# Kernel tuning notes

Hardware: AMD Instinct MI355X
Metric: run time of the kernel (lower is better)

Reference implementation:

```python
import jax, jax.numpy as jnp
import numpy as np

B, T, N, D, H, F, L, V = 4, 512, 1024, 384, 8, 1536, 6, 8000
HD = D // H


def _pe(t, d):
    pos = np.arange(t)[:, None].astype(np.float32)
    div = np.exp(np.arange(0, d, 2).astype(np.float32) * (-np.log(10000.0) / d))
    pe = np.zeros((t, d), np.float32)
    pe[:, 0::2] = np.sin(pos * div)
    pe[:, 1::2] = np.cos(pos * div)
    return jnp.asarray(pe)


def _ln(x, g, b, eps=1e-5):
    m = jnp.mean(x, -1, keepdims=True)
    v = jnp.mean((x - m) ** 2, -1, keepdims=True)
    return (x - m) * jax.lax.rsqrt(v + eps) * g + b


def _mha(xq, xkv, qw, qb, kw, kb, vw, vb, ow, ob, causal):
    Bq, Tq, Dm = xq.shape
    Nk = xkv.shape[1]

    def proj(x, w, b):
        return (x @ w + b).reshape(x.shape[0], x.shape[1], H, HD).transpose(0, 2, 1, 3)

    q, k, v = proj(xq, qw, qb), proj(xkv, kw, kb), proj(xkv, vw, vb)
    s = jnp.einsum('bhtd,bhnd->bhtn', q, k) * (HD ** -0.5)
    if causal:  # triu(ones(T, T_total), diagonal=1) since T_total == T (no cache)
        mask = jnp.triu(jnp.ones((Tq, Nk), bool), 1)
        s = jnp.where(mask, -jnp.inf, s)
    p = jax.nn.softmax(s, -1)
    o = jnp.einsum('bhtn,bhnd->bhtd', p, v).transpose(0, 2, 1, 3).reshape(Bq, Tq, Dm)
    return o @ ow + ob


def setup_inputs() -> dict:
    key = jax.random.key(0)
    ks = iter(jax.random.split(key, 40))
    w = lambda shape, s=0.02: jax.random.normal(next(ks), shape, jnp.float32) * s
    inp = {
        'encoder_out': jax.random.normal(next(ks), (B, N, D), jnp.float32),
        'emb': w((V, D)),
    }
    for p in ('sa', 'ca'):
        for n in ('q', 'k', 'v', 'o'):
            inp[f'{p}_{n}w'] = w((L, D, D))
            inp[f'{p}_{n}b'] = jnp.zeros((L, D), jnp.float32)
    for n in ('ln1', 'ln2', 'ln3'):
        inp[f'{n}_g'] = jnp.ones((L, D), jnp.float32)
        inp[f'{n}_b'] = jnp.zeros((L, D), jnp.float32)
    inp['ffn_w1'] = w((L, D, F)); inp['ffn_b1'] = jnp.zeros((L, F), jnp.float32)
    inp['ffn_w2'] = w((L, F, D)); inp['ffn_b2'] = jnp.zeros((L, D), jnp.float32)
    inp['on_g'] = jnp.ones((D,), jnp.float32); inp['on_b'] = jnp.zeros((D,), jnp.float32)
    inp['out_w'] = w((D, V)); inp['out_b'] = jnp.zeros((V,), jnp.float32)
    inp['target_ids'] = jax.random.randint(next(ks), (B, T), 0, V)
    return inp


def _forward(encoder_out, emb, sa_qw, sa_qb, sa_kw, sa_kb, sa_vw, sa_vb, sa_ow, sa_ob,
             ca_qw, ca_qb, ca_kw, ca_kb, ca_vw, ca_vb, ca_ow, ca_ob,
             ln1_g, ln1_b, ln2_g, ln2_b, ln3_g, ln3_b,
             ffn_w1, ffn_b1, ffn_w2, ffn_b2, on_g, on_b, out_w, out_b, target_ids):
    x = emb[target_ids] + _pe(T, D)[None]  # [B,T,D]
    for i in range(L):
        a = _mha(x, x, sa_qw[i], sa_qb[i], sa_kw[i], sa_kb[i], sa_vw[i], sa_vb[i], sa_ow[i], sa_ob[i], True)
        x = _ln(x + a, ln1_g[i], ln1_b[i])
        c = _mha(x, encoder_out, ca_qw[i], ca_qb[i], ca_kw[i], ca_kb[i], ca_vw[i], ca_vb[i], ca_ow[i], ca_ob[i], False)
        x = _ln(x + c, ln2_g[i], ln2_b[i])
        h = jax.nn.gelu(x @ ffn_w1[i] + ffn_b1[i], approximate=False) @ ffn_w2[i] + ffn_b2[i]
        x = _ln(x + h, ln3_g[i], ln3_b[i])
    x = _ln(x, on_g, on_b)
    return x @ out_w + out_b  # logits [B,T,V]


def reference(encoder_out, emb, sa_qw, sa_qb, sa_kw, sa_kb, sa_vw, sa_vb, sa_ow, sa_ob,
              ca_qw, ca_qb, ca_kw, ca_kb, ca_vw, ca_vb, ca_ow, ca_ob,
              ln1_g, ln1_b, ln2_g, ln2_b, ln3_g, ln3_b,
              ffn_w1, ffn_b1, ffn_w2, ffn_b2, on_g, on_b, out_w, out_b, target_ids):
    return _forward(encoder_out, emb, sa_qw, sa_qb, sa_kw, sa_kb, sa_vw, sa_vb, sa_ow, sa_ob,
                    ca_qw, ca_qb, ca_kw, ca_kb, ca_vw, ca_vb, ca_ow, ca_ob,
                    ln1_g, ln1_b, ln2_g, ln2_b, ln3_g, ln3_b,
                    ffn_w1, ffn_b1, ffn_w2, ffn_b2, on_g, on_b, out_w, out_b, target_ids)
```

## Files before the change

### kernel.cpp

```cpp
#include <hip/hip_runtime.h>
#include <hip/hip_bf16.h>
#include <math.h>

typedef __hip_bfloat16 bf16;
typedef __attribute__((ext_vector_type(8))) short short8;
typedef __attribute__((ext_vector_type(4))) float f32x4;
typedef __attribute__((ext_vector_type(4))) unsigned short us4;

#define Bc 4
#define Tc 512
#define Nc 1024
#define Dc 384
#define Hc 8
#define Fc 1536
#define Lc 6
#define Vc 8000
#define HDc 48

__device__ __forceinline__ float ldsel(const void* p, long long i, int isbf) {
  return isbf ? __bfloat162float(((const bf16*)p)[i]) : ((const float*)p)[i];
}
__device__ __forceinline__ void stsel(void* p, long long i, float v, int isbf) {
  if (isbf) ((bf16*)p)[i] = __float2bfloat16(v);
  else      ((float*)p)[i] = v;
}
__device__ __forceinline__ unsigned short f2bf(float x) {
  unsigned int u = __float_as_uint(x);
  return (unsigned short)((u + 0x7fffu + ((u >> 16) & 1u)) >> 16);
}

__global__ void detect_kernel(const unsigned int* __restrict__ g,
                              int* __restrict__ flag) {
  if (threadIdx.x == 0 && blockIdx.x == 0)
    *flag = (g[0] == 0x3F803F80u) ? 1 : 0;
}

__global__ __launch_bounds__(256) void wt_kernel(
    const void* __restrict__ in, bf16* __restrict__ out, int K, int N,
    long long outStride, const int* __restrict__ flagp) {
  const int isbf = *flagp;
  __shared__ float t[32][33];
  const long long cin = (long long)blockIdx.z * K * N;
  const long long cout = (long long)blockIdx.z * outStride;
  const int n0 = blockIdx.x * 32, k0 = blockIdx.y * 32;
  const int tx = threadIdx.x, ty = threadIdx.y;
#pragma unroll
  for (int r = 0; r < 4; ++r)
    t[ty * 4 + r][tx] =
        ldsel(in, cin + (long long)(k0 + ty * 4 + r) * N + n0 + tx, isbf);
  __syncthreads();
#pragma unroll
  for (int r = 0; r < 4; ++r)
    out[cout + (long long)(n0 + ty * 4 + r) * K + k0 + tx] =
        __float2bfloat16(t[tx][ty * 4 + r]);
}

__global__ __launch_bounds__(256) void cvt_kernel(
    const void* __restrict__ in, bf16* __restrict__ out,
    const int* __restrict__ flagp) {
  const int isbf = *flagp;
  const long long i = ((long long)blockIdx.x * 256 + threadIdx.x) * 4;
  if (isbf) {
    *(us4*)((unsigned short*)out + i) = *(const us4*)((const unsigned short*)in + i);
  } else {
    float4 v = *(const float4*)((const float*)in + i);
    unsigned short* o = (unsigned short*)out + i;
    o[0] = f2bf(v.x); o[1] = f2bf(v.y); o[2] = f2bf(v.z); o[3] = f2bf(v.w);
  }
}

__global__ __launch_bounds__(256) void bfuse_kernel(
    const void* __restrict__ b0, const void* __restrict__ b1,
    const void* __restrict__ b2, float* __restrict__ out, int nseg,
    const int* __restrict__ flagp) {
  const int isbf = *flagp;
  const int i = blockIdx.x;
  for (int n = threadIdx.x; n < Dc; n += 256) {
    out[(long long)i * nseg * Dc + n] = ldsel(b0, (long long)i * Dc + n, isbf);
    if (nseg > 1)
      out[(long long)i * nseg * Dc + Dc + n] = ldsel(b1, (long long)i * Dc + n, isbf);
    if (nseg > 2)
      out[(long long)i * nseg * Dc + 2 * Dc + n] = ldsel(b2, (long long)i * Dc + n, isbf);
  }
}

__global__ __launch_bounds__(256) void mgemm_kernel(
    const bf16* __restrict__ A, const void* __restrict__ B, long long bOff,
    const void* __restrict__ bias, long long biasOff, void* __restrict__ C,
    int M, int N, int K, int cMode, int act, int biasBf, int bT,
    const int* __restrict__ flagp) {
  const int isbf = *flagp;
  const int cbf = (cMode == 2) ? isbf : cMode;
  const int bbf = (biasBf == 2) ? isbf : biasBf;

  __shared__ __align__(16) unsigned short As[64][72];
  __shared__ __align__(16) unsigned short Bs[64][72];

  const int tid = threadIdx.x;
  const int m0 = blockIdx.x * 64, n0 = blockIdx.y * 64;
  const int lane = tid & 63, wv = tid >> 6;
  const int fr = lane & 15;
  const int fk = (lane >> 4) * 8;

  const int sr = tid >> 2;
  const int sk = (tid & 3) * 16;

  f32x4 acc[4] = {};

  if (bT == 0) {
    const bf16* Bp = (const bf16*)B + bOff;
    const bf16* Ar = A + (long long)(m0 + sr) * K + sk;
    const bf16* Br = Bp + (long long)(n0 + sr) * K + sk;
    short8 a0 = *(const short8*)(Ar);
    short8 a1 = *(const short8*)(Ar + 8);
    short8 b0 = *(const short8*)(Br);
    short8 b1 = *(const short8*)(Br + 8);
    for (int k0 = 0; k0 < K; k0 += 64) {
      *(short8*)(&As[sr][sk]) = a0;
      *(short8*)(&As[sr][sk + 8]) = a1;
      *(short8*)(&Bs[sr][sk]) = b0;
      *(short8*)(&Bs[sr][sk + 8]) = b1;
      __syncthreads();
      if (k0 + 64 < K) {
        a0 = *(const short8*)(Ar + k0 + 64);
        a1 = *(const short8*)(Ar + k0 + 72);
        b0 = *(const short8*)(Br + k0 + 64);
        b1 = *(const short8*)(Br + k0 + 72);
      }
#pragma unroll
      for (int ks = 0; ks < 64; ks += 32) {
        short8 a = *(const short8*)(&As[16 * wv + fr][ks + fk]);
#pragma unroll
        for (int j = 0; j < 4; ++j) {
          short8 b = *(const short8*)(&Bs[16 * j + fr][ks + fk]);
          acc[j] = __builtin_amdgcn_mfma_f32_16x16x32_bf16(a, b, acc[j], 0, 0, 0);
        }
      }
      __syncthreads();
    }
  } else {
    const int bk = tid >> 2;
    const int bn = (tid & 3) * 16;
    for (int k0 = 0; k0 < K; k0 += 64) {
      {
        const long long off = (long long)(m0 + sr) * K + k0 + sk;
        const short8* p = (const short8*)(A + off);
        *(short8*)(&As[sr][sk]) = p[0];
        *(short8*)(&As[sr][sk + 8]) = p[1];
      }
      const long long off = bOff + (long long)(k0 + bk) * N + n0 + bn;
      if (isbf) {
        const short8* p = (const short8*)((const bf16*)B + off);
        short8 v0 = p[0], v1 = p[1];
#pragma unroll
        for (int j = 0; j < 8; ++j) {
          Bs[bn + j][bk] = (unsigned short)v0[j];
          Bs[bn + 8 + j][bk] = (unsigned short)v1[j];
        }
      } else {
        const float4* p = (const float4*)((const float*)B + off);
        float4 f0 = p[0], f1 = p[1], f2 = p[2], f3 = p[3];
        Bs[bn + 0][bk] = f2bf(f0.x);  Bs[bn + 1][bk] = f2bf(f0.y);
        Bs[bn + 2][bk] = f2bf(f0.z);  Bs[bn + 3][bk] = f2bf(f0.w);
        Bs[bn + 4][bk] = f2bf(f1.x);  Bs[bn + 5][bk] = f2bf(f1.y);
        Bs[bn + 6][bk] = f2bf(f1.z);  Bs[bn + 7][bk] = f2bf(f1.w);
        Bs[bn + 8][bk] = f2bf(f2.x);  Bs[bn + 9][bk] = f2bf(f2.y);
        Bs[bn + 10][bk] = f2bf(f2.z); Bs[bn + 11][bk] = f2bf(f2.w);
        Bs[bn + 12][bk] = f2bf(f3.x); Bs[bn + 13][bk] = f2bf(f3.y);
        Bs[bn + 14][bk] = f2bf(f3.z); Bs[bn + 15][bk] = f2bf(f3.w);
      }
      __syncthreads();
#pragma unroll
      for (int ks = 0; ks < 64; ks += 32) {
        short8 a = *(const short8*)(&As[16 * wv + fr][ks + fk]);
#pragma unroll
        for (int j = 0; j < 4; ++j) {
          short8 b = *(const short8*)(&Bs[16 * j + fr][ks + fk]);
          acc[j] = __builtin_amdgcn_mfma_f32_16x16x32_bf16(a, b, acc[j], 0, 0, 0);
        }
      }
      __syncthreads();
    }
  }

#pragma unroll
  for (int j = 0; j < 4; ++j) {
    const int col = n0 + 16 * j + fr;
    float bv = bias ? ldsel(bias, biasOff + col, bbf) : 0.f;
#pragma unroll
    for (int q = 0; q < 4; ++q) {
      const int row = m0 + 16 * wv + (lane >> 4) * 4 + q;
      float v = acc[j][q] + bv;
      if (act == 1) v = 0.5f * v * (1.f + erff(v * 0.70710678118654752f));
      stsel(C, (long long)row * N + col, v, cbf);
    }
  }
}

__global__ __launch_bounds__(256) void mattn_kernel(
    const bf16* __restrict__ Qb, int ldq, const bf16* __restrict__ Kb,
    const bf16* __restrict__ Vb, int ldkv, int kvRows,
    float* __restrict__ PO, float* __restrict__ Mb, float* __restrict__ Lb,
    int Nk, int causal) {
  const int bh = blockIdx.y;
  const int b = bh >> 3, h = bh & 7;
  const int row0 = blockIdx.x * 64;
  const int z = blockIdx.z;
  const int tid = threadIdx.x;
  const int lane = tid & 63, wv = tid >> 6;
  const int fr = lane & 15, g = lane >> 4;
  const int fk = g * 8, g4 = g * 4;
  const int rbase = row0 + wv * 16 + g4;

  __shared__ __align__(16) unsigned short Ks[64][72];
  __shared__ __align__(16) unsigned short Vt[48][72];
  __shared__ __align__(16) unsigned short Ps[4][16][72];

  for (int i = tid; i < 64 * 16; i += 256) Ks[i >> 4][48 + (i & 15)] = 0;

  const int qrow = row0 + wv * 16 + fr;
  const bf16* Qp = Qb + (long long)(b * Tc + qrow) * ldq + h * HDc;
  short8 q0 = *(const short8*)(Qp + fk);
  short8 q1 = {};
  if (g < 2) q1 = *(const short8*)(Qp + 32 + fk);

  const bf16* Kp = Kb + (long long)b * kvRows * ldkv + h * HDc;
  const bf16* Vp = Vb + (long long)b * kvRows * ldkv + h * HDc;

  const int c0 = tid, c1 = 256 + tid;
  const int r0 = c0 / 6, o0 = (c0 % 6) * 8;
  const int r1 = c1 / 6, o1 = (c1 % 6) * 8;
  const bool has1 = (tid < 128);

  const int nT = causal ? (blockIdx.x + 1) : (Nk >> 6);
  const int tlo = (nT * z) >> 1, thi = (nT * (z + 1)) >> 1;

  float m[4] = {-3e38f, -3e38f, -3e38f, -3e38f};
  float l[4] = {0.f, 0.f, 0.f, 0.f};
  f32x4 oa[3] = {};

  short8 kA = {}, vA = {}, kB = {}, vB = {};
  if (tlo < thi) {
    const long long nb = (long long)tlo * 64;
    kA = *(const short8*)(Kp + (nb + r0) * ldkv + o0);
    vA = *(const short8*)(Vp + (nb + r0) * ldkv + o0);
    if (has1) {
      kB = *(const short8*)(Kp + (nb + r1) * ldkv + o1);
      vB = *(const short8*)(Vp + (nb + r1) * ldkv + o1);
    }
  }

  const float scale = 0.14433756729740643f;

  for (int t = tlo; t < thi; ++t) {
    *(short8*)&Ks[r0][o0] = kA;
#pragma unroll
    for (int j = 0; j < 8; ++j) Vt[o0 + j][r0] = (unsigned short)vA[j];
    if (has1) {
      *(short8*)&Ks[r1][o1] = kB;
#pragma unroll
      for (int j = 0; j < 8; ++j) Vt[o1 + j][r1] = (unsigned short)vB[j];
    }
    __syncthreads();

    if (t + 1 < thi) {
      const long long nb = (long long)(t + 1) * 64;
      kA = *(const short8*)(Kp + (nb + r0) * ldkv + o0);
      vA = *(const short8*)(Vp + (nb + r0) * ldkv + o0);
      if (has1) {
        kB = *(const short8*)(Kp + (nb + r1) * ldkv + o1);
        vB = *(const short8*)(Vp + (nb + r1) * ldkv + o1);
      }
    }

    f32x4 s[4] = {};
#pragma unroll
    for (int tt = 0; tt < 4; ++tt) {
      short8 b0 = *(const short8*)&Ks[16 * tt + fr][fk];
      short8 b1 = *(const short8*)&Ks[16 * tt + fr][32 + fk];
      s[tt] = __builtin_amdgcn_mfma_f32_16x16x32_bf16(q0, b0, s[tt], 0, 0, 0);
      s[tt] = __builtin_amdgcn_mfma_f32_16x16x32_bf16(q1, b1, s[tt], 0, 0, 0);
    }

    const int n0 = t * 64;
#pragma unroll
    for (int tt = 0; tt < 4; ++tt) {
      const int n = n0 + 16 * tt + fr;
#pragma unroll
      for (int q = 0; q < 4; ++q) {
        float v = s[tt][q] * scale;
        if (causal && n > rbase + q) v = -3e38f;
        s[tt][q] = v;
      }
    }

#pragma unroll
    for (int q = 0; q < 4; ++q) {
      float tm = fmaxf(fmaxf(s[0][q], s[1][q]), fmaxf(s[2][q], s[3][q]));
      tm = fmaxf(tm, __shfl_xor(tm, 1, 64));
      tm = fmaxf(tm, __shfl_xor(tm, 2, 64));
      tm = fmaxf(tm, __shfl_xor(tm, 4, 64));
      tm = fmaxf(tm, __shfl_xor(tm, 8, 64));
      const float mn = fmaxf(m[q], tm);
      const float f = expf(m[q] - mn);
      float rs = 0.f;
#pragma unroll
      for (int tt = 0; tt < 4; ++tt) {
        float p = expf(s[tt][q] - mn);
        s[tt][q] = p;
        rs += p;
      }
      rs += __shfl_xor(rs, 1, 64);
      rs += __shfl_xor(rs, 2, 64);
      rs += __shfl_xor(rs, 4, 64);
      rs += __shfl_xor(rs, 8, 64);
      l[q] = l[q] * f + rs;
      m[q] = mn;
      oa[0][q] *= f;
      oa[1][q] *= f;
      oa[2][q] *= f;
    }

#pragma unroll
    for (int tt = 0; tt < 4; ++tt)
#pragma unroll
      for (int q = 0; q < 4; ++q)
        Ps[wv][g4 + q][16 * tt + fr] = f2bf(s[tt][q]);

#pragma unroll
    for (int ks = 0; ks < 64; ks += 32) {
      short8 a = *(const short8*)&Ps[wv][fr][ks + fk];
#pragma unroll
      for (int jd = 0; jd < 3; ++jd) {
        short8 bv = *(const short8*)&Vt[16 * jd + fr][ks + fk];
        oa[jd] = __builtin_amdgcn_mfma_f32_16x16x32_bf16(a, bv, oa[jd], 0, 0, 0);
      }
    }
    __syncthreads();
  }

#pragma unroll
  for (int q = 0; q < 4; ++q) {
    float* pp = PO + (long long)(z * (Bc * Tc) + b * Tc + rbase + q) * Dc + h * HDc;
#pragma unroll
    for (int jd = 0; jd < 3; ++jd) pp[16 * jd + fr] = oa[jd][q];
    if (fr == 0) {
      const int mi = z * (Bc * Hc * Tc) + (bh << 9) + rbase + q;
      Mb[mi] = m[q];
      Lb[mi] = l[q];
    }
  }
}

__global__ __launch_bounds__(384) void acomb_kernel(
    const float* __restrict__ PO, const float* __restrict__ Mb,
    const float* __restrict__ Lb, bf16* __restrict__ ATT) {
  const int row = blockIdx.x;
  const int d = threadIdx.x;
  const int b = row >> 9, t = row & 511;
  const int h = d / HDc;
  const int mi = ((b << 3) + h) * Tc + t;
  const float m0 = Mb[mi], m1 = Mb[Bc * Hc * Tc + mi];
  const float l0 = Lb[mi], l1 = Lb[Bc * Hc * Tc + mi];
  const float M = fmaxf(m0, m1);
  const float w0 = expf(m0 - M), w1 = expf(m1 - M);
  const float L = w0 * l0 + w1 * l1;
  const float o = (w0 * PO[(long long)row * Dc + d] +
                   w1 * PO[(long long)(Bc * Tc + row) * Dc + d]) / L;
  ATT[(long long)row * Dc + d] = __float2bfloat16(o);
}

__global__ __launch_bounds__(256) void ln_kernel(
    const float* __restrict__ X, const float* __restrict__ R,
    const void* __restrict__ g, const void* __restrict__ bta, long long gOff,
    void* __restrict__ Y, int yMode, bf16* __restrict__ Yb,
    const int* __restrict__ flagp) {
  const int isbf = *flagp;
  long long row = blockIdx.x;
  int tid = threadIdx.x;
  const float* xr = X + row * Dc;
  const float* rr = R ? R + row * Dc : nullptr;
  float v0 = xr[tid] + (rr ? rr[tid] : 0.f);
  float v1 = 0.f;
  if (tid < 128) v1 = xr[256 + tid] + (rr ? rr[256 + tid] : 0.f);
  __shared__ float red[256];
  red[tid] = v0 + v1;
  __syncthreads();
  for (int s = 128; s > 0; s >>= 1) {
    if (tid < s) red[tid] += red[tid + s];
    __syncthreads();
  }
  float mean = red[0] * (1.f / 384.f);
  __syncthreads();
  float d0 = v0 - mean;
  float d1 = (tid < 128) ? (v1 - mean) : 0.f;
  red[tid] = d0 * d0 + d1 * d1;
  __syncthreads();
  for (int s = 128; s > 0; s >>= 1) {
    if (tid < s) red[tid] += red[tid + s];
    __syncthreads();
  }
  float rstd = rsqrtf(red[0] * (1.f / 384.f) + 1e-5f);
  long long yoff = row * Dc;
  float y0 = d0 * rstd * ldsel(g, gOff + tid, isbf) + ldsel(bta, gOff + tid, isbf);
  stsel(Y, yoff + tid, y0, yMode);
  if (Yb) Yb[yoff + tid] = __float2bfloat16(y0);
  if (tid < 128) {
    float y1 = d1 * rstd * ldsel(g, gOff + 256 + tid, isbf) +
               ldsel(bta, gOff + 256 + tid, isbf);
    stsel(Y, yoff + 256 + tid, y1, yMode);
    if (Yb) Yb[yoff + 256 + tid] = __float2bfloat16(y1);
  }
}

__global__ __launch_bounds__(384) void embed_kernel(
    const void* __restrict__ emb, const int* __restrict__ ids,
    float* __restrict__ X, bf16* __restrict__ Xb,
    const int* __restrict__ flagp) {
  const int isbf = *flagp;
  long long row = blockIdx.x;
  int t = (int)(row % Tc);
  int d = threadIdx.x;
  int id = ids[row];
  float e = ldsel(emb, (long long)id * Dc + d, isbf);
  int i2 = d & ~1;
  float div = expf((float)i2 * (-9.210340371976184f / 384.f));
  float ang = (float)t * div;
  float pe = (d & 1) ? cosf(ang) : sinf(ang);
  float v = e + pe;
  X[row * Dc + d] = v;
  Xb[row * Dc + d] = __float2bfloat16(v);
}

extern "C" void kernel_launch(void* const* d_in, const int* in_sizes, int n_in,
                              void* d_out, int out_size, void* d_ws,
                              size_t ws_size, hipStream_t stream) {
  (void)in_sizes; (void)n_in; (void)out_size;

  const void* enc = d_in[0];
  const void* emb = d_in[1];
  const void* sa_w[4]; const void* sa_b[4];
  for (int j = 0; j < 4; ++j) { sa_w[j] = d_in[2 + 2 * j]; sa_b[j] = d_in[3 + 2 * j]; }
  const void* ca_w[4]; const void* ca_b[4];
  for (int j = 0; j < 4; ++j) { ca_w[j] = d_in[10 + 2 * j]; ca_b[j] = d_in[11 + 2 * j]; }
  const void* ln_g[3]; const void* ln_b[3];
  for (int j = 0; j < 3; ++j) { ln_g[j] = d_in[18 + 2 * j]; ln_b[j] = d_in[19 + 2 * j]; }
  const void* fw1 = d_in[24];
  const void* fb1 = d_in[25];
  const void* fw2 = d_in[26];
  const void* fb2 = d_in[27];
  const void* ong = d_in[28];
  const void* onb = d_in[29];
  const void* outw = d_in[30];
  const void* outb = d_in[31];
  const int* ids = (const int*)d_in[32];

  char* ob = (char*)d_out;
  float* X   = (float*)ob;
  bf16* Xb   = (bf16*)(ob + 3145728);
  float* AO  = (float*)(ob + 4718592);
  bf16* QKV  = (bf16*)(ob + 7864320);
  bf16* KVca = (bf16*)(ob + 12582912);
  bf16* ATT  = (bf16*)(ob + 18874368);
  bf16* HID  = (bf16*)(ob + 20447232);
  float* PO  = (float*)(ob + 20447232);
  float* Mb  = (float*)(ob + 26738688);
  float* Lb  = (float*)(ob + 26869760);
  bf16* encB = (bf16*)(ob + 27000832);
  float* bQKV = (float*)(ob + 30146560);
  float* bKVc = (float*)(ob + 30174208);

  bf16* Y = (bf16*)d_ws;
  int* flag = (int*)((char*)d_ws + 1572864);

  const bool bigws = (ws_size >= (size_t)36028672);
  char* wtb = (char*)d_ws + 1573120;
  bf16* saQKVT = (bf16*)(wtb + 0);
  bf16* saOT   = (bf16*)(wtb + 5308416);
  bf16* caQT   = (bf16*)(wtb + 7077888);
  bf16* caKVT  = (bf16*)(wtb + 8847360);
  bf16* caOT   = (bf16*)(wtb + 12386304);
  bf16* f1T    = (bf16*)(wtb + 14155776);
  bf16* f2T    = (bf16*)(wtb + 21233664);
  bf16* outT   = (bf16*)(wtb + 28311552);

  const int BT = Bc * Tc;
  const int F32 = 0, BF16 = 1, FLAG = 2;

  detect_kernel<<<dim3(1), dim3(64), 0, stream>>>((const unsigned int*)ln_g[0], flag);

  if (bigws) {
    auto wt = [&](const void* in, bf16* out, int K, int N, long long ostr, int C) {
      wt_kernel<<<dim3(N / 32, K / 32, C), dim3(32, 8), 0, stream>>>(
          in, out, K, N, ostr, flag);
    };
    wt(sa_w[0], saQKVT, 384, 384, 1152LL * 384, Lc);
    wt(sa_w[1], saQKVT + 147456, 384, 384, 1152LL * 384, Lc);
    wt(sa_w[2], saQKVT + 294912, 384, 384, 1152LL * 384, Lc);
    wt(sa_w[3], saOT, 384, 384, 147456, Lc);
    wt(ca_w[0], caQT, 384, 384, 147456, Lc);
    wt(ca_w[1], caKVT, 384, 384, 294912, Lc);
    wt(ca_w[2], caKVT + 147456, 384, 384, 294912, Lc);
    wt(ca_w[3], caOT, 384, 384, 147456, Lc);
    wt(fw1, f1T, 384, 1536, 589824, Lc);
    wt(fw2, f2T, 1536, 384, 589824, Lc);
    wt(outw, outT, 384, 8000, 0, 1);
    bfuse_kernel<<<dim3(Lc), dim3(256), 0, stream>>>(sa_b[0], sa_b[1], sa_b[2],
                                                     bQKV, 3, flag);
    bfuse_kernel<<<dim3(Lc), dim3(256), 0, stream>>>(ca_b[1], ca_b[2], ca_b[2],
                                                     bKVc, 2, flag);
  }
  cvt_kernel<<<dim3(1536), dim3(256), 0, stream>>>(enc, encB, flag);

  auto gemmT = [&](const bf16* A, const bf16* Bt, long long bOff,
                   const void* bias, long long biasOff, int biasBf, void* C,
                   int M, int N, int K, int cM, int act) {
    mgemm_kernel<<<dim3(M / 64, N / 64), dim3(256), 0, stream>>>(
        A, Bt, bOff, bias, biasOff, C, M, N, K, cM, act, biasBf, 0, flag);
  };
  auto gemmO = [&](const bf16* A, const void* Bo, long long bOff,
                   const void* bias, long long biasOff, void* C,
                   int M, int N, int K, int cM, int act) {
    mgemm_kernel<<<dim3(M / 64, N / 64), dim3(256), 0, stream>>>(
        A, Bo, bOff, bias, biasOff, C, M, N, K, cM, act, FLAG, 1, flag);
  };
  auto ln = [&](const float* Xp, const float* Rp, const void* g,
                const void* b, long long gOff, void* Yp, int yMode, bf16* Yb) {
    ln_kernel<<<dim3(BT), dim3(256), 0, stream>>>(Xp, Rp, g, b, gOff, Yp,
                                                  yMode, Yb, flag);
  };
  auto attn = [&](const bf16* Q, int ldq, const bf16* Kp, const bf16* Vp,
                  int ldkv, int kvRows, int Nk, int causal) {
    mattn_kernel<<<dim3(Tc / 64, Bc * Hc, 2), dim3(256), 0, stream>>>(
        Q, ldq, Kp, Vp, ldkv, kvRows, PO, Mb, Lb, Nk, causal);
    acomb_kernel<<<dim3(BT), dim3(384), 0, stream>>>(PO, Mb, Lb, ATT);
  };

  embed_kernel<<<dim3(BT), dim3(384), 0, stream>>>(emb, ids, X, Xb, flag);

  bf16* Qf = QKV;
  bf16* Kf = KVca;
  bf16* Vf = (bf16*)((char*)KVca + 3145728);

  for (int i = 0; i < Lc; ++i) {
    const long long wD = (long long)i * Dc * Dc;
    const long long bD = (long long)i * Dc;

    if (bigws) {
      gemmT(Xb, saQKVT, (long long)i * 1152 * 384, bQKV, (long long)i * 1152,
            F32, QKV, BT, 1152, 384, BF16, 0);
      attn(QKV, 1152, QKV + 384, QKV + 768, 1152, Tc, Tc, 1);
      gemmT(ATT, saOT, wD, sa_b[3], bD, FLAG, AO, BT, Dc, Dc, F32, 0);
    } else {
      gemmO(Xb, sa_w[0], wD, sa_b[0], bD, Qf, BT, Dc, Dc, BF16, 0);
      gemmO(Xb, sa_w[1], wD, sa_b[1], bD, Kf, BT, Dc, Dc, BF16, 0);
      gemmO(Xb, sa_w[2], wD, sa_b[2], bD, Vf, BT, Dc, Dc, BF16, 0);
      attn(Qf, 384, Kf, Vf, 384, Tc, Tc, 1);
      gemmO(ATT, sa_w[3], wD, sa_b[3], bD, AO, BT, Dc, Dc, F32, 0);
    }
    ln(X, AO, ln_g[0], ln_b[0], bD, X, F32, Xb);

    if (bigws) {
      gemmT(Xb, caQT, wD, ca_b[0], bD, FLAG, QKV, BT, Dc, Dc, BF16, 0);
      gemmT(encB, caKVT, (long long)i * 768 * 384, bKVc, (long long)i * 768,
            F32, KVca, Bc * Nc, 768, 384, BF16, 0);
      attn(QKV, 384, KVca, KVca + 384, 768, Nc, Nc, 0);
      gemmT(ATT, caOT, wD, ca_b[3], bD, FLAG, AO, BT, Dc, Dc, F32, 0);
    } else {
      gemmO(Xb, ca_w[0], wD, ca_b[0], bD, Qf, BT, Dc, Dc, BF16, 0);
      gemmO(encB, ca_w[1], wD, ca_b[1], bD, Kf, Bc * Nc, Dc, Dc, BF16, 0);
      gemmO(encB, ca_w[2], wD, ca_b[2], bD, Vf, Bc * Nc, Dc, Dc, BF16, 0);
      attn(Qf, 384, Kf, Vf, 384, Nc, Nc, 0);
      gemmO(ATT, ca_w[3], wD, ca_b[3], bD, AO, BT, Dc, Dc, F32, 0);
    }
    ln(X, AO, ln_g[1], ln_b[1], bD, X, F32, Xb);

    if (bigws) {
      gemmT(Xb, f1T, (long long)i * 1536 * 384, fb1, (long long)i * Fc, FLAG,
            HID, BT, Fc, Dc, BF16, 1 );
      gemmT(HID, f2T, (long long)i * 384 * 1536, fb2, bD, FLAG, AO,
            BT, Dc, Fc, F32, 0);
    } else {
      gemmO(Xb, fw1, (long long)i * Dc * Fc, fb1, (long long)i * Fc, HID,
            BT, Fc, Dc, BF16, 1);
      gemmO(HID, fw2, (long long)i * Fc * Dc, fb2, bD, AO, BT, Dc, Fc, F32, 0);
    }
    ln(X, AO, ln_g[2], ln_b[2], bD, X, F32, Xb);
  }

  ln(X, nullptr, ong, onb, 0, Y, BF16, nullptr);
  if (bigws)
    gemmT(Y, outT, 0, outb, 0, FLAG, d_out, BT, Vc, Dc, FLAG, 0);
  else
    gemmO(Y, outw, 0, outb, 0, d_out, BT, Vc, Dc, FLAG, 0);
}
```

Baseline: 1.058 ms.

## Add 128-row MFMA GEMM, fuse attention combine into O-proj, warp-per-row layernorm

Adds a templated GEMM with 128x128 and 128x64 tiles for the large QKV, cross-attention KV, FFN1 and output projections, giving more data reuse per block. Removes the separate split-KV combine kernel: the output-projection GEMM now merges the two partial attention results while loading its A tile. The attention softmax switches to exp2f with a log2e-scaled constant. LayerNorm is rewritten to use one wavefront per row with shuffle reductions and single-pass mean and variance, which may lose some precision. The combine-fused GEMM recomputes the merge weights per tile and uses the slower scalar LDS path, and the larger tiles launch fewer blocks.

Result: slower. 1.154 ms (+9.0%).

```diff
diff --git a/kernel.cpp b/kernel.cpp
--- a/kernel.cpp
+++ b/kernel.cpp
@@ -84,11 +84,97 @@
   }
 }
 
+template <int BN>
+__global__ __launch_bounds__(256) void mgemm128_kernel(
+    const bf16* __restrict__ A, const bf16* __restrict__ Bt, long long bOff,
+    const void* __restrict__ bias, long long biasOff, void* __restrict__ C,
+    int M, int N, int K, int cMode, int act, int biasBf,
+    const int* __restrict__ flagp) {
+  constexpr int RN = BN / 32;
+  const int isbf = *flagp;
+  const int cbf = (cMode == 2) ? isbf : cMode;
+  const int bbf = (biasBf == 2) ? isbf : biasBf;
+
+  __shared__ __align__(16) unsigned short As[128][72];
+  __shared__ __align__(16) unsigned short Bs[BN][72];
+
+  const int tid = threadIdx.x;
+  const int m0 = blockIdx.x * 128, n0 = blockIdx.y * BN;
+  const int lane = tid & 63, wv = tid >> 6;
+  const int wm = wv >> 1, wn = wv & 1;
+  const int fr = lane & 15;
+  const int fk = (lane >> 4) * 8;
+
+  const int ar = tid >> 3;
+  const int ac = (tid & 7) * 8;
+  const bf16* Ap = A + (long long)(m0 + ar) * K + ac;
+  const bf16* Bp = Bt + bOff + (long long)(n0 + ar) * K + ac;
+
+  short8 pa[4], pb[RN * 2];
+#pragma unroll
+  for (int r = 0; r < 4; ++r) pa[r] = *(const short8*)(Ap + r * 32 * K);
+#pragma unroll
+  for (int r = 0; r < RN * 2; ++r) pb[r] = *(const short8*)(Bp + r * 32 * K);
+
+  f32x4 acc[4][RN] = {};
+
+  for (int k0 = 0; k0 < K; k0 += 64) {
+#pragma unroll
+    for (int r = 0; r < 4; ++r) *(short8*)(&As[ar + 32 * r][ac]) = pa[r];
+#pragma unroll
+    for (int r = 0; r < RN * 2; ++r) *(short8*)(&Bs[ar + 32 * r][ac]) = pb[r];
+    __syncthreads();
+    if (k0 + 64 < K) {
+#pragma unroll
+      for (int r = 0; r < 4; ++r)
+        pa[r] = *(const short8*)(Ap + r * 32 * K + k0 + 64);
+#pragma unroll
+      for (int r = 0; r < RN * 2; ++r)
+        pb[r] = *(const short8*)(Bp + r * 32 * K + k0 + 64);
+    }
+#pragma unroll
+    for (int ks = 0; ks < 64; ks += 32) {
+      short8 af[4];
+#pragma unroll
+      for (int mi = 0; mi < 4; ++mi)
+        af[mi] = *(const short8*)(&As[wm * 64 + mi * 16 + fr][ks + fk]);
+      short8 bg[RN];
+#pragma unroll
+      for (int ni = 0; ni < RN; ++ni)
+        bg[ni] = *(const short8*)(&Bs[wn * (BN / 2) + ni * 16 + fr][ks + fk]);
+#pragma unroll
+      for (int mi = 0; mi < 4; ++mi)
+#pragma unroll
+        for (int ni = 0; ni < RN; ++ni)
+          acc[mi][ni] =
+              __builtin_amdgcn_mfma_f32_16x16x32_bf16(af[mi], bg[ni], acc[mi][ni], 0, 0, 0);
+    }
+    __syncthreads();
+  }
+
+#pragma unroll
+  for (int ni = 0; ni < RN; ++ni) {
+    const int col = n0 + wn * (BN / 2) + ni * 16 + fr;
+    const float bv = bias ? ldsel(bias, biasOff + col, bbf) : 0.f;
+#pragma unroll
+    for (int mi = 0; mi < 4; ++mi) {
+#pragma unroll
+      for (int q = 0; q < 4; ++q) {
+        const int row = m0 + wm * 64 + mi * 16 + (lane >> 4) * 4 + q;
+        float v = acc[mi][ni][q] + bv;
+        if (act == 1) v = 0.5f * v * (1.f + erff(v * 0.70710678118654752f));
+        stsel(C, (long long)row * N + col, v, cbf);
+      }
+    }
+  }
+}
+
 __global__ __launch_bounds__(256) void mgemm_kernel(
     const bf16* __restrict__ A, const void* __restrict__ B, long long bOff,
     const void* __restrict__ bias, long long biasOff, void* __restrict__ C,
     int M, int N, int K, int cMode, int act, int biasBf, int bT,
-    const int* __restrict__ flagp) {
+    const float* __restrict__ POm, const float* __restrict__ Mst,
+    const float* __restrict__ Lst, int comb, const int* __restrict__ flagp) {
   const int isbf = *flagp;
   const int cbf = (cMode == 2) ? isbf : cMode;
   const int bbf = (biasBf == 2) ? isbf : biasBf;
@@ -107,7 +193,7 @@
 
   f32x4 acc[4] = {};
 
-  if (bT == 0) {
+  if (bT == 0 && comb == 0) {
     const bf16* Bp = (const bf16*)B + bOff;
     const bf16* Ar = A + (long long)(m0 + sr) * K + sk;
     const bf16* Br = Bp + (long long)(n0 + sr) * K + sk;
@@ -142,32 +228,62 @@
     const int bk = tid >> 2;
     const int bn = (tid & 3) * 16;
     for (int k0 = 0; k0 < K; k0 += 64) {
-      {
+      if (comb) {
+        const int gm = m0 + sr;
+        const int gk = k0 + sk;
+        const int hh = gk / 48;
+        const int bb = gm >> 9, tt = gm & 511;
+        const int mi = ((bb << 3) + hh) * 512 + tt;
+        const float ma = Mst[mi], mb2 = Mst[16384 + mi];
+        const float la = Lst[mi], lb2 = Lst[16384 + mi];
+        const float MM = fmaxf(ma, mb2);
+        float w0 = exp2f(ma - MM), w1 = exp2f(mb2 - MM);
+        const float invL = 1.f / (w0 * la + w1 * lb2);
+        w0 *= invL; w1 *= invL;
+        const float* p0 = POm + (long long)gm * Dc + gk;
+        const float* p1 = POm + (long long)(2048 + gm) * Dc + gk;
+#pragma unroll
+        for (int e = 0; e < 16; e += 4) {
+          float4 x0 = *(const float4*)(p0 + e);
+          float4 x1 = *(const float4*)(p1 + e);
+          As[sr][sk + e + 0] = f2bf(w0 * x0.x + w1 * x1.x);
+          As[sr][sk + e + 1] = f2bf(w0 * x0.y + w1 * x1.y);
+          As[sr][sk + e + 2] = f2bf(w0 * x0.z + w1 * x1.z);
+          As[sr][sk + e + 3] = f2bf(w0 * x0.w + w1 * x1.w);
+        }
+      } else {
         const long long off = (long long)(m0 + sr) * K + k0 + sk;
         const short8* p = (const short8*)(A + off);
         *(short8*)(&As[sr][sk]) = p[0];
         *(short8*)(&As[sr][sk + 8]) = p[1];
       }
-      const long long off = bOff + (long long)(k0 + bk) * N + n0 + bn;
-      if (isbf) {
+      if (bT == 0) {
+        const long long off = bOff + (long long)(n0 + sr) * K + k0 + sk;
         const short8* p = (const short8*)((const bf16*)B + off);
-        short8 v0 = p[0], v1 = p[1];
-#pragma unroll
-        for (int j = 0; j < 8; ++j) {
-          Bs[bn + j][bk] = (unsigned short)v0[j];
-          Bs[bn + 8 + j][bk] = (unsigned short)v1[j];
+        *(short8*)(&Bs[sr][sk]) = p[0];
+        *(short8*)(&Bs[sr][sk + 8]) = p[1];
+      } else {
+        const long long off = bOff + (long long)(k0 + bk) * N + n0 + bn;
+        if (isbf) {
+          const short8* p = (const short8*)((const bf16*)B + off);
+          short8 v0 = p[0], v1 = p[1];
+#pragma unroll
+          for (int j = 0; j < 8; ++j) {
+            Bs[bn + j][bk] = (unsigned short)v0[j];
+            Bs[bn + 8 + j][bk] = (unsigned short)v1[j];
+          }
+        } else {
+          const float4* p = (const float4*)((const float*)B + off);
+          float4 f0 = p[0], f1 = p[1], f2 = p[2], f3 = p[3];
+          Bs[bn + 0][bk] = f2bf(f0.x);  Bs[bn + 1][bk] = f2bf(f0.y);
+          Bs[bn + 2][bk] = f2bf(f0.z);  Bs[bn + 3][bk] = f2bf(f0.w);
+          Bs[bn + 4][bk] = f2bf(f1.x);  Bs[bn + 5][bk] = f2bf(f1.y);
+          Bs[bn + 6][bk] = f2bf(f1.z);  Bs[bn + 7][bk] = f2bf(f1.w);
+          Bs[bn + 8][bk] = f2bf(f2.x);  Bs[bn + 9][bk] = f2bf(f2.y);
+          Bs[bn + 10][bk] = f2bf(f2.z); Bs[bn + 11][bk] = f2bf(f2.w);
+          Bs[bn + 12][bk] = f2bf(f3.x); Bs[bn + 13][bk] = f2bf(f3.y);
+          Bs[bn + 14][bk] = f2bf(f3.z); Bs[bn + 15][bk] = f2bf(f3.w);
         }
-      } else {
-        const float4* p = (const float4*)((const float*)B + off);
-        float4 f0 = p[0], f1 = p[1], f2 = p[2], f3 = p[3];
-        Bs[bn + 0][bk] = f2bf(f0.x);  Bs[bn + 1][bk] = f2bf(f0.y);
-        Bs[bn + 2][bk] = f2bf(f0.z);  Bs[bn + 3][bk] = f2bf(f0.w);
-        Bs[bn + 4][bk] = f2bf(f1.x);  Bs[bn + 5][bk] = f2bf(f1.y);
-        Bs[bn + 6][bk] = f2bf(f1.z);  Bs[bn + 7][bk] = f2bf(f1.w);
-        Bs[bn + 8][bk] = f2bf(f2.x);  Bs[bn + 9][bk] = f2bf(f2.y);
-        Bs[bn + 10][bk] = f2bf(f2.z); Bs[bn + 11][bk] = f2bf(f2.w);
-        Bs[bn + 12][bk] = f2bf(f3.x); Bs[bn + 13][bk] = f2bf(f3.y);
-        Bs[bn + 14][bk] = f2bf(f3.z); Bs[bn + 15][bk] = f2bf(f3.w);
       }
       __syncthreads();
 #pragma unroll
@@ -250,7 +366,7 @@
     }
   }
 
-  const float scale = 0.14433756729740643f;
+  const float scale = 0.20823509f;
 
   for (int t = tlo; t < thi; ++t) {
     *(short8*)&Ks[r0][o0] = kA;
@@ -302,11 +418,11 @@
       tm = fmaxf(tm, __shfl_xor(tm, 4, 64));
       tm = fmaxf(tm, __shfl_xor(tm, 8, 64));
       const float mn = fmaxf(m[q], tm);
-      const float f = expf(m[q] - mn);
+      const float f = exp2f(m[q] - mn);
       float rs = 0.f;
 #pragma unroll
       for (int tt = 0; tt < 4; ++tt) {
-        float p = expf(s[tt][q] - mn);
+        float p = exp2f(s[tt][q] - mn);
         s[tt][q] = p;
         rs += p;
       }
@@ -352,64 +468,40 @@
   }
 }
 
-__global__ __launch_bounds__(384) void acomb_kernel(
-    const float* __restrict__ PO, const float* __restrict__ Mb,
-    const float* __restrict__ Lb, bf16* __restrict__ ATT) {
-  const int row = blockIdx.x;
-  const int d = threadIdx.x;
-  const int b = row >> 9, t = row & 511;
-  const int h = d / HDc;
-  const int mi = ((b << 3) + h) * Tc + t;
-  const float m0 = Mb[mi], m1 = Mb[Bc * Hc * Tc + mi];
-  const float l0 = Lb[mi], l1 = Lb[Bc * Hc * Tc + mi];
-  const float M = fmaxf(m0, m1);
-  const float w0 = expf(m0 - M), w1 = expf(m1 - M);
-  const float L = w0 * l0 + w1 * l1;
-  const float o = (w0 * PO[(long long)row * Dc + d] +
-                   w1 * PO[(long long)(Bc * Tc + row) * Dc + d]) / L;
-  ATT[(long long)row * Dc + d] = __float2bfloat16(o);
-}
-
-__global__ __launch_bounds__(256) void ln_kernel(
+__global__ __launch_bounds__(256) void lnw_kernel(
     const float* __restrict__ X, const float* __restrict__ R,
     const void* __restrict__ g, const void* __restrict__ bta, long long gOff,
     void* __restrict__ Y, int yMode, bf16* __restrict__ Yb,
     const int* __restrict__ flagp) {
   const int isbf = *flagp;
-  long long row = blockIdx.x;
-  int tid = threadIdx.x;
+  const long long row = blockIdx.x * 4 + (threadIdx.x >> 6);
+  const int lane = threadIdx.x & 63;
   const float* xr = X + row * Dc;
   const float* rr = R ? R + row * Dc : nullptr;
-  float v0 = xr[tid] + (rr ? rr[tid] : 0.f);
-  float v1 = 0.f;
-  if (tid < 128) v1 = xr[256 + tid] + (rr ? rr[256 + tid] : 0.f);
-  __shared__ float red[256];
-  red[tid] = v0 + v1;
-  __syncthreads();
-  for (int s = 128; s > 0; s >>= 1) {
-    if (tid < s) red[tid] += red[tid + s];
-    __syncthreads();
-  }
-  float mean = red[0] * (1.f / 384.f);
-  __syncthreads();
-  float d0 = v0 - mean;
-  float d1 = (tid < 128) ? (v1 - mean) : 0.f;
-  red[tid] = d0 * d0 + d1 * d1;
-  __syncthreads();
-  for (int s = 128; s > 0; s >>= 1) {
-    if (tid < s) red[tid] += red[tid + s];
-    __syncthreads();
-  }
-  float rstd = rsqrtf(red[0] * (1.f / 384.f) + 1e-5f);
-  long long yoff = row * Dc;
-  float y0 = d0 * rstd * ldsel(g, gOff + tid, isbf) + ldsel(bta, gOff + tid, isbf);
-  stsel(Y, yoff + tid, y0, yMode);
-  if (Yb) Yb[yoff + tid] = __float2bfloat16(y0);
-  if (tid < 128) {
-    float y1 = d1 * rstd * ldsel(g, gOff + 256 + tid, isbf) +
-               ldsel(bta, gOff + 256 + tid, isbf);
-    stsel(Y, yoff + 256 + tid, y1, yMode);
-    if (Yb) Yb[yoff + 256 + tid] = __float2bfloat16(y1);
+  float v[6];
+  float s = 0.f, s2 = 0.f;
+#pragma unroll
+  for (int j = 0; j < 6; ++j) {
+    const int d = lane + 64 * j;
+    float x = xr[d] + (rr ? rr[d] : 0.f);
+    v[j] = x; s += x; s2 += x * x;
+  }
+#pragma unroll
+  for (int k = 1; k < 64; k <<= 1) {
+    s += __shfl_xor(s, k, 64);
+    s2 += __shfl_xor(s2, k, 64);
+  }
+  const float mean = s * (1.f / 384.f);
+  const float var = s2 * (1.f / 384.f) - mean * mean;
+  const float rstd = rsqrtf(var + 1e-5f);
+  const long long yo = row * Dc;
+#pragma unroll
+  for (int j = 0; j < 6; ++j) {
+    const int d = lane + 64 * j;
+    float y = (v[j] - mean) * rstd * ldsel(g, gOff + d, isbf) +
+              ldsel(bta, gOff + d, isbf);
+    stsel(Y, yo + d, y, yMode);
+    if (Yb) Yb[yo + d] = __float2bfloat16(y);
   }
 }
 
@@ -461,7 +553,6 @@
   float* AO  = (float*)(ob + 4718592);
   bf16* QKV  = (bf16*)(ob + 7864320);
   bf16* KVca = (bf16*)(ob + 12582912);
-  bf16* ATT  = (bf16*)(ob + 18874368);
   bf16* HID  = (bf16*)(ob + 20447232);
   float* PO  = (float*)(ob + 20447232);
   float* Mb  = (float*)(ob + 26738688);
@@ -512,28 +603,34 @@
   }
   cvt_kernel<<<dim3(1536), dim3(256), 0, stream>>>(enc, encB, flag);
 
-  auto gemmT = [&](const bf16* A, const bf16* Bt, long long bOff,
-                   const void* bias, long long biasOff, int biasBf, void* C,
-                   int M, int N, int K, int cM, int act) {
+  auto gemm128 = [&](const bf16* A, const bf16* Bt, long long bOff,
+                     const void* bias, long long biasOff, int biasBf, void* C,
+                     int M, int N, int K, int cM, int act) {
+    mgemm128_kernel<128><<<dim3(M / 128, N / 128), dim3(256), 0, stream>>>(
+        A, Bt, bOff, bias, biasOff, C, M, N, K, cM, act, biasBf, flag);
+  };
+  auto gemm128n64 = [&](const bf16* A, const bf16* Bt, long long bOff,
+                        const void* bias, long long biasOff, int biasBf,
+                        void* C, int M, int N, int K, int cM, int act) {
+    mgemm128_kernel<64><<<dim3(M / 128, N / 64), dim3(256), 0, stream>>>(
+        A, Bt, bOff, bias, biasOff, C, M, N, K, cM, act, biasBf, flag);
+  };
+  auto gemmOld = [&](const bf16* A, const void* Bo, long long bOff,
+                     const void* bias, long long biasOff, int biasBf, void* C,
+                     int M, int N, int K, int cM, int act, int bT, int comb) {
     mgemm_kernel<<<dim3(M / 64, N / 64), dim3(256), 0, stream>>>(
-        A, Bt, bOff, bias, biasOff, C, M, N, K, cM, act, biasBf, 0, flag);
-  };
-  auto gemmO = [&](const bf16* A, const void* Bo, long long bOff,
-                   const void* bias, long long biasOff, void* C,
-                   int M, int N, int K, int cM, int act) {
-    mgemm_kernel<<<dim3(M / 64, N / 64), dim3(256), 0, stream>>>(
-        A, Bo, bOff, bias, biasOff, C, M, N, K, cM, act, FLAG, 1, flag);
+        A, Bo, bOff, bias, biasOff, C, M, N, K, cM, act, biasBf, bT,
+        PO, Mb, Lb, comb, flag);
   };
   auto ln = [&](const float* Xp, const float* Rp, const void* g,
                 const void* b, long long gOff, void* Yp, int yMode, bf16* Yb) {
-    ln_kernel<<<dim3(BT), dim3(256), 0, stream>>>(Xp, Rp, g, b, gOff, Yp,
-                                                  yMode, Yb, flag);
+    lnw_kernel<<<dim3(BT / 4), dim3(256), 0, stream>>>(Xp, Rp, g, b, gOff, Yp,
+                                                       yMode, Yb, flag);
   };
   auto attn = [&](const bf16* Q, int ldq, const bf16* Kp, const bf16* Vp,
                   int ldkv, int kvRows, int Nk, int causal) {
     mattn_kernel<<<dim3(Tc / 64, Bc * Hc, 2), dim3(256), 0, stream>>>(
         Q, ldq, Kp, Vp, ldkv, kvRows, PO, Mb, Lb, Nk, causal);
-    acomb_kernel<<<dim3(BT), dim3(384), 0, stream>>>(PO, Mb, Lb, ATT);
   };
 
   embed_kernel<<<dim3(BT), dim3(384), 0, stream>>>(emb, ids, X, Xb, flag);
@@ -547,50 +644,51 @@
     const long long bD = (long long)i * Dc;
 
     if (bigws) {
-      gemmT(Xb, saQKVT, (long long)i * 1152 * 384, bQKV, (long long)i * 1152,
-            F32, QKV, BT, 1152, 384, BF16, 0);
+      gemm128(Xb, saQKVT, (long long)i * 1152 * 384, bQKV, (long long)i * 1152,
+              F32, QKV, BT, 1152, 384, BF16, 0);
       attn(QKV, 1152, QKV + 384, QKV + 768, 1152, Tc, Tc, 1);
-      gemmT(ATT, saOT, wD, sa_b[3], bD, FLAG, AO, BT, Dc, Dc, F32, 0);
+      gemmOld(nullptr, saOT, wD, sa_b[3], bD, FLAG, AO, BT, Dc, Dc, F32, 0, 0, 1);
     } else {
-      gemmO(Xb, sa_w[0], wD, sa_b[0], bD, Qf, BT, Dc, Dc, BF16, 0);
-      gemmO(Xb, sa_w[1], wD, sa_b[1], bD, Kf, BT, Dc, Dc, BF16, 0);
-      gemmO(Xb, sa_w[2], wD, sa_b[2], bD, Vf, BT, Dc, Dc, BF16, 0);
+      gemmOld(Xb, sa_w[0], wD, sa_b[0], bD, FLAG, Qf, BT, Dc, Dc, BF16, 0, 1, 0);
+      gemmOld(Xb, sa_w[1], wD, sa_b[1], bD, FLAG, Kf, BT, Dc, Dc, BF16, 0, 1, 0);
+      gemmOld(Xb, sa_w[2], wD, sa_b[2], bD, FLAG, Vf, BT, Dc, Dc, BF16, 0, 1, 0);
       attn(Qf, 384, Kf, Vf, 384, Tc, Tc, 1);
-      gemmO(ATT, sa_w[3], wD, sa_b[3], bD, AO, BT, Dc, Dc, F32, 0);
+      gemmOld(nullptr, sa_w[3], wD, sa_b[3], bD, FLAG, AO, BT, Dc, Dc, F32, 0, 1, 1);
     }
     ln(X, AO, ln_g[0], ln_b[0], bD, X, F32, Xb);
 
     if (bigws) {
-      gemmT(Xb, caQT, wD, ca_b[0], bD, FLAG, QKV, BT, Dc, Dc, BF16, 0);
-      gemmT(encB, caKVT, (long long)i * 768 * 384, bKVc, (long long)i * 768,
-            F32, KVca, Bc * Nc, 768, 384, BF16, 0);
+      gemmOld(Xb, caQT, wD, ca_b[0], bD, FLAG, QKV, BT, Dc, Dc, BF16, 0, 0, 0);
+      gemm128(encB, caKVT, (long long)i * 768 * 384, bKVc, (long long)i * 768,
+              F32, KVca, Bc * Nc, 768, 384, BF16, 0);
       attn(QKV, 384, KVca, KVca + 384, 768, Nc, Nc, 0);
-      gemmT(ATT, caOT, wD, ca_b[3], bD, FLAG, AO, BT, Dc, Dc, F32, 0);
+      gemmOld(nullptr, caOT, wD, ca_b[3], bD, FLAG, AO, BT, Dc, Dc, F32, 0, 0, 1);
     } else {
-      gemmO(Xb, ca_w[0], wD, ca_b[0], bD, Qf, BT, Dc, Dc, BF16, 0);
-      gemmO(encB, ca_w[1], wD, ca_b[1], bD, Kf, Bc * Nc, Dc, Dc, BF16, 0);
-      gemmO(encB, ca_w[2], wD, ca_b[2], bD, Vf, Bc * Nc, Dc, Dc, BF16, 0);
+      gemmOld(Xb, ca_w[0], wD, ca_b[0], bD, FLAG, Qf, BT, Dc, Dc, BF16, 0, 1, 0);
+      gemmOld(encB, ca_w[1], wD, ca_b[1], bD, FLAG, Kf, Bc * Nc, Dc, Dc, BF16, 0, 1, 0);
+      gemmOld(encB, ca_w[2], wD, ca_b[2], bD, FLAG, Vf, Bc * Nc, Dc, Dc, BF16, 0, 1, 0);
       attn(Qf, 384, Kf, Vf, 384, Nc, Nc, 0);
-      gemmO(ATT, ca_w[3], wD, ca_b[3], bD, AO, BT, Dc, Dc, F32, 0);
+      gemmOld(nullptr, ca_w[3], wD, ca_b[3], bD, FLAG, AO, BT, Dc, Dc, F32, 0, 1, 1);
     }
     ln(X, AO, ln_g[1], ln_b[1], bD, X, F32, Xb);
 
     if (bigws) {
-      gemmT(Xb, f1T, (long long)i * 1536 * 384, fb1, (long long)i * Fc, FLAG,
-            HID, BT, Fc, Dc, BF16, 1 );
-      gemmT(HID, f2T, (long long)i * 384 * 1536, fb2, bD, FLAG, AO,
-            BT, Dc, Fc, F32, 0);
+      gemm128(Xb, f1T, (long long)i * 1536 * 384, fb1, (long long)i * Fc, FLAG,
+              HID, BT, Fc, Dc, BF16, 1 );
+      gemmOld(HID, f2T, (long long)i * 384 * 1536, fb2, bD, FLAG, AO,
+              BT, Dc, Fc, F32, 0, 0, 0);
     } else {
-      gemmO(Xb, fw1, (long long)i * Dc * Fc, fb1, (long long)i * Fc, HID,
-            BT, Fc, Dc, BF16, 1);
-      gemmO(HID, fw2, (long long)i * Fc * Dc, fb2, bD, AO, BT, Dc, Fc, F32, 0);
+      gemmOld(Xb, fw1, (long long)i * Dc * Fc, fb1, (long long)i * Fc, FLAG,
+              HID, BT, Fc, Dc, BF16, 1, 1, 0);
+      gemmOld(HID, fw2, (long long)i * Fc * Dc, fb2, bD, FLAG, AO,
+              BT, Dc, Fc, F32, 0, 1, 0);
     }
     ln(X, AO, ln_g[2], ln_b[2], bD, X, F32, Xb);
   }
 
   ln(X, nullptr, ong, onb, 0, Y, BF16, nullptr);
   if (bigws)
-    gemmT(Y, outT, 0, outb, 0, FLAG, d_out, BT, Vc, Dc, FLAG, 0);
+    gemm128n64(Y, outT, 0, outb, 0, FLAG, d_out, BT, Vc, Dc, FLAG, 0);
   else
-    gemmO(Y, outw, 0, outb, 0, d_out, BT, Vc, Dc, FLAG, 0);
-}
+    gemmOld(Y, outw, 0, outb, 0, FLAG, d_out, BT, Vc, Dc, FLAG, 0, 1, 0);
+}
```
